# Kernel optimization log

Hardware: AMD Instinct MI355X
Metric: run time of the kernel (lower is better)

Reference implementation:

```python
import math
import jax, jax.numpy as jnp
import numpy as np

BLOCK = 32          # MRA block size (fixed to 32 by the CUDA kernels)
NUM_HEADS = 12
HEAD_DIM = 64
NUM_BLOCKS = 512    # top-k blocks kept per (batch*head) row
FIRST_N = 0         # initial_prior_first_n_blocks
DIAG_N = 3          # initial_prior_diagonal_n_blocks


def _low_res_logit(q, k, v, mask):
    # q,k,v: (B, S, D); mask: (B, S)
    B, S, D = q.shape
    nb = S // BLOCK
    tc = mask.reshape(B, nb, BLOCK).sum(-1)            # token count per block
    denom = tc[:, :, None] + 1e-6
    q_hat = q.reshape(B, nb, BLOCK, D).sum(2) / denom
    k_hat = k.reshape(B, nb, BLOCK, D).sum(2) / denom
    v_hat = v.reshape(B, nb, BLOCK, D).sum(2) / denom
    logit = jnp.einsum('bnd,bmd->bnm', q_hat, k_hat) / math.sqrt(D)
    row_max = logit.max(-1, keepdims=True)             # before mask penalty, as in torch
    logit = logit - 1e4 * ((tc[:, None, :] * tc[:, :, None]) < 0.5).astype(logit.dtype)
    return logit, tc, row_max, v_hat


def _block_idxes(lrl):
    # lrl: (B, nb, nb) normalized low-res logits (stop-gradient'ed by caller)
    B, nb, _ = lrl.shape
    if DIAG_N > 0:
        off = DIAG_N // 2
        r = jnp.arange(nb)
        diag = (jnp.abs(r[:, None] - r[None, :]) <= off).astype(lrl.dtype)
        lrl = lrl + diag[None] * 5000.0
    if FIRST_N > 0:
        lrl = lrl.at[:, :FIRST_N, :].add(5000.0)
        lrl = lrl.at[:, :, :FIRST_N].add(5000.0)
    vals, idx = jax.lax.top_k(lrl.reshape(B, -1), NUM_BLOCKS)
    thresh = vals.min(-1)
    hi_mask = (lrl >= thresh[:, None, None]).astype(lrl.dtype)
    return idx, hi_mask


def mra2_attention(q, k, v, mask):
    # q,k,v: (meta_batch, S, D); mask: (meta_batch, S). approx_mode == 'full'.
    B, S, D = q.shape
    nb = S // BLOCK
    q = q * mask[:, :, None]
    k = k * mask[:, :, None]
    v = v * mask[:, :, None]
    lrl, tc, row_max, v_hat = _low_res_logit(q, k, v, mask)
    idx, hi_mask = _block_idxes(jax.lax.stop_gradient(lrl - row_max))
    qi = idx // nb                                     # (B, NUM_BLOCKS) query block id
    ki = idx % nb                                      # (B, NUM_BLOCKS) key block id
    b_ix = jnp.arange(B)[:, None]
    # mm_to_sparse: gather blocks, block layout is (key_pos, query_pos) as in the CUDA kernel
    qb = q.reshape(B, nb, BLOCK, D)[b_ix, qi]          # (B, NB, 32, D)
    kb = k.reshape(B, nb, BLOCK, D)[b_ix, ki]
    hr_logit = jnp.einsum('bnkd,bnqd->bnkq', kb, qb) / math.sqrt(D)
    # sparse_max: per-query-row max over all selected blocks in that row
    idx_vals = hr_logit.max(-2)                        # (B, NB, 32q)
    max_vals = jnp.full((B, nb, BLOCK), -1e9, hr_logit.dtype).at[b_ix, qi].max(idx_vals)
    hr_logit = hr_logit - max_vals[b_ix, qi][:, :, None, :]
    # sparse_mask over key positions of each selected block
    mk = mask.reshape(B, nb, BLOCK)[b_ix, ki]          # (B, NB, 32k)
    hr_logit = hr_logit - 1e4 * (1.0 - mk)[:, :, :, None]
    hr_attn = jnp.exp(hr_logit)
    # sparse_dense_mm: scatter-add block contributions back to query rows
    vb = v.reshape(B, nb, BLOCK, D)[b_ix, ki]
    out_blk = jnp.einsum('bnkq,bnkd->bnqd', hr_attn, vb)
    hr_out = jnp.zeros((B, nb, BLOCK, D), q.dtype).at[b_ix, qi].add(out_blk).reshape(B, S, D)
    hr_norm = jnp.zeros((B, nb, BLOCK), q.dtype).at[b_ix, qi].add(hr_attn.sum(-2)).reshape(B, S)
    max_vals_flat = max_vals.reshape(B, S)
    # low-resolution branch (approx_mode == 'full')
    lr_attn = jnp.exp(lrl - row_max - 1e4 * hi_mask) * tc[:, None, :]
    lr_out = jnp.broadcast_to(
        jnp.einsum('bnm,bmd->bnd', lr_attn, v_hat)[:, :, None, :], (B, nb, BLOCK, D)
    ).reshape(B, S, D)
    lr_norm = jnp.broadcast_to(lr_attn.sum(-1)[:, :, None], (B, nb, BLOCK)).reshape(B, S)
    log_corr = (jnp.broadcast_to(row_max, (B, nb, BLOCK)).reshape(B, S) - max_vals_flat) * mask
    lr_corr = jnp.exp(log_corr * (log_corr <= 0).astype(log_corr.dtype))
    hr_corr = jnp.exp(-log_corr * (log_corr > 0).astype(log_corr.dtype))
    num = hr_out * hr_corr[:, :, None] + lr_out * lr_corr[:, :, None]
    den = hr_norm * hr_corr + lr_norm * lr_corr + 1e-6
    ctx = num / den[:, :, None]
    return ctx * mask[:, :, None]


def setup_inputs() -> dict:
    key = jax.random.key(0)
    ks = jax.random.split(key, 4)
    B, S, H = 4, 4096, 768
    return {
        'hidden_states': jax.random.normal(ks[0], (B, S, H), jnp.float32),
        'attention_mask': jnp.zeros((B, S), jnp.float32),  # extended mask form (0 == keep)
        'Wq': jax.random.normal(ks[1], (H, H), jnp.float32) * 0.02,
        'bq': jnp.zeros((H,), jnp.float32),
        'Wk': jax.random.normal(ks[2], (H, H), jnp.float32) * 0.02,
        'bk': jnp.zeros((H,), jnp.float32),
        'Wv': jax.random.normal(ks[3], (H, H), jnp.float32) * 0.02,
        'bv': jnp.zeros((H,), jnp.float32),
    }


def reference(hidden_states, attention_mask, Wq, bq, Wk, bk, Wv, bv):
    B, S, H = hidden_states.shape

    def heads(x):  # (B,S,H) -> (B*nh, S, hd)
        return x.reshape(B, S, NUM_HEADS, HEAD_DIM).transpose(0, 2, 1, 3).reshape(B * NUM_HEADS, S, HEAD_DIM)

    q = heads(hidden_states @ Wq.T + bq)
    k = heads(hidden_states @ Wk.T + bk)
    v = heads(hidden_states @ Wv.T + bv)
    # revert get_extended_attention_mask: (1 - m) * -10000 -> m
    mask = 1.0 + attention_mask / 10000.0
    mask = jnp.broadcast_to(mask[:, None, :], (B, NUM_HEADS, S)).reshape(B * NUM_HEADS, S)
    ctx = mra2_attention(q, k, v, mask)
    return ctx.reshape(B, NUM_HEADS, S, HEAD_DIM).transpose(0, 2, 1, 3).reshape(B, S, H)
```

## Files before the change

### kernel.cpp

```cpp
#include <hip/hip_runtime.h>
#include <math.h>


#define S_LEN 4096
#define NBLK  128
#define BHT   48
#define HD    64

typedef __attribute__((ext_vector_type(8))) short bf16x8;
typedef __attribute__((ext_vector_type(4))) float f32x4;
typedef unsigned short u16;
typedef unsigned int   u32;
typedef unsigned long long u64;

__device__ __forceinline__ u16 bf16rne(float x) {
    u32 u = __float_as_uint(x);
    u32 r = u + 0x7FFFu + ((u >> 16) & 1u);
    return (u16)(r >> 16);
}
__device__ __forceinline__ float b2f(u16 h) {
    return __uint_as_float((u32)h << 16);
}

__device__ __forceinline__ void gload_lds16(const void* g, void* l) {
    __builtin_amdgcn_global_load_lds((const __attribute__((address_space(1))) void*)g,
                                     (__attribute__((address_space(3))) void*)l, 16, 0, 0);
}

__global__ __launch_bounds__(256) void split_kernel(
    const float* __restrict__ x, u16* __restrict__ hi, u16* __restrict__ lo, int n8)
{
    int i = blockIdx.x * 256 + threadIdx.x;
    if (i >= n8) return;
    const float4* xp = (const float4*)x + (size_t)i * 2;
    float4 a = xp[0], b = xp[1];
    float xs[8] = {a.x, a.y, a.z, a.w, b.x, b.y, b.z, b.w};
    bf16x8 vh, vl;
    #pragma unroll
    for (int j = 0; j < 8; ++j) {
        u16 hh = bf16rne(xs[j]);
        float hf = b2f(hh);
        vh[j] = (short)hh;
        vl[j] = (short)bf16rne(xs[j] - hf);
    }
    *(bf16x8*)&hi[(size_t)i * 8] = vh;
    *(bf16x8*)&lo[(size_t)i * 8] = vl;
}

__global__ __launch_bounds__(256, 3) void qkv_mfma(
    const u16* __restrict__ Xh, const u16* __restrict__ Xl,
    const u16* __restrict__ Wh, const u16* __restrict__ Wl,
    const float* __restrict__ bq, const float* __restrict__ bk, const float* __restrict__ bv,
    const float* __restrict__ am,
    u16* __restrict__ Qh, u16* __restrict__ Ql,
    u16* __restrict__ Kh, u16* __restrict__ Kl,
    u16* __restrict__ Vth, u16* __restrict__ Vtl)
{
    const int wg = blockIdx.x;
    const int logical = (wg & 7) * 288 + (wg >> 3);
    const int mt = logical / 18;
    const int rr = logical - mt * 18;
    const int nt = rr % 6;
    const int z  = rr / 6;

    const float* bias = (z == 0) ? bq : (z == 1) ? bk : bv;
    const u16* Wzh = Wh + (size_t)z * 768 * 768;
    const u16* Wzl = Wl + (size_t)z * 768 * 768;
    const int m0 = mt * 128, n0 = nt * 128;

    __shared__ char smem[16896];
    const int tid  = threadIdx.x;
    const int lane = tid & 63;
    const int w    = tid >> 6;
    const int wm   = (w >> 1) * 64, wn = (w & 1) * 64;

    const int rbase = (w < 2) ? m0 : n0;
    const int sub0  = (w & 1) * 4;
    char* ldsdst    = (w < 2) ? smem : (smem + 8192);
    const int srow = lane >> 2;
    const int scg  = (lane & 3) ^ ((lane >> 3) & 3);
    const int tslot = (lane & 15) * 4 + ((lane >> 4) ^ ((lane >> 1) & 3));

    f32x4 acc[4][4];
    #pragma unroll
    for (int i = 0; i < 4; ++i)
        #pragma unroll
        for (int j = 0; j < 4; ++j) acc[i][j] = (f32x4){0.f, 0.f, 0.f, 0.f};

    for (int k0 = 0; k0 < 2304; k0 += 32) {
        const u16* srcA = (k0 < 1536) ? Xh : Xl;
        const u16* srcB = (k0 < 768) ? Wzh : ((k0 < 1536) ? Wzl : Wzh);
        const int  kk   = (k0 < 768) ? k0 : ((k0 < 1536) ? (k0 - 768) : (k0 - 1536));
        const u16* src  = (w < 2) ? srcA : srcB;
        __syncthreads();
        #pragma unroll
        for (int i = 0; i < 4; ++i) {
            const u16* g = src + (size_t)(rbase + (sub0 + i) * 16 + srow) * 768 + (kk + scg * 8);
            gload_lds16(g, ldsdst + (sub0 + i) * 1024);
        }
        __syncthreads();

        bf16x8 af[4], bf[4];
        #pragma unroll
        for (int f = 0; f < 4; ++f) {
            af[f] = *(const bf16x8*)&smem[0    + ((w >> 1) * 4 + f) * 1024 + tslot * 16];
            bf[f] = *(const bf16x8*)&smem[8192 + ((w & 1)  * 4 + f) * 1024 + tslot * 16];
        }
        #pragma unroll
        for (int i = 0; i < 4; ++i)
            #pragma unroll
            for (int j = 0; j < 4; ++j)
                acc[i][j] = __builtin_amdgcn_mfma_f32_16x16x32_bf16(af[i], bf[j], acc[i][j], 0, 0, 0);
    }

    if (z < 2) {
        u16* Ph = (z == 0) ? Qh : Kh;
        u16* Pl = (z == 0) ? Ql : Kl;
        const float qscale = (z == 0) ? 0.125f : 1.0f;
        #pragma unroll
        for (int i = 0; i < 4; ++i) {
            #pragma unroll
            for (int j = 0; j < 4; ++j) {
                int col = n0 + wn + j * 16 + (lane & 15);
                int h = col >> 6, d = col & 63;
                float bsv = bias[col];
                #pragma unroll
                for (int r = 0; r < 4; ++r) {
                    int row = m0 + wm + i * 16 + (lane >> 4) * 4 + r;
                    int b = row >> 12, s = row & 4095;
                    float mv = 1.0f + am[row] * 1e-4f;
                    float e = (acc[i][j][r] + bsv) * mv * qscale;
                    u16 hh = bf16rne(e);
                    u16 ll = bf16rne(e - b2f(hh));
                    size_t a = (((size_t)(b * 12 + h)) * S_LEN + s) * HD + d;
                    Ph[a] = hh; Pl[a] = ll;
                }
            }
        }
    } else {
        u32* buf = (u32*)smem;
        const int bb = m0 >> 12;
        #pragma unroll
        for (int p = 0; p < 4; ++p) {
            const int hh_ = p & 1;
            const int rh  = p >> 1;
            __syncthreads();
            if (((w & 1) == hh_) && ((w >> 1) == rh)) {
                #pragma unroll
                for (int i = 0; i < 4; ++i) {
                    #pragma unroll
                    for (int j = 0; j < 4; ++j) {
                        int d_local = j * 16 + (lane & 15);
                        int col = n0 + hh_ * 64 + d_local;
                        float bsv = bias[col];
                        #pragma unroll
                        for (int r = 0; r < 4; ++r) {
                            int s_local = i * 16 + (lane >> 4) * 4 + r;
                            float mv = 1.0f + am[m0 + rh * 64 + s_local] * 1e-4f;
                            float e = (acc[i][j][r] + bsv) * mv;
                            u16 h16 = bf16rne(e);
                            u16 l16 = bf16rne(e - b2f(h16));
                            buf[d_local * 66 + s_local] = ((u32)h16 << 16) | (u32)l16;
                        }
                    }
                }
            }
            __syncthreads();
            int d_local = tid >> 2;
            int s_chunk = (tid & 3) * 16;
            int head = (n0 >> 6) + hh_;
            size_t ob = (((size_t)(bb * 12 + head)) * HD + d_local) * S_LEN
                        + (m0 & 4095) + rh * 64 + s_chunk;
            #pragma unroll
            for (int gq = 0; gq < 2; ++gq) {
                bf16x8 vh8, vl8;
                #pragma unroll
                for (int t = 0; t < 8; ++t) {
                    u32 pk = buf[d_local * 66 + s_chunk + gq * 8 + t];
                    vh8[t] = (short)(pk >> 16);
                    vl8[t] = (short)(pk & 0xFFFF);
                }
                *(bf16x8*)&Vth[ob + gq * 8] = vh8;
                *(bf16x8*)&Vtl[ob + gq * 8] = vl8;
            }
        }
    }
}

__global__ __launch_bounds__(256) void hsum_kernel(
    const float* __restrict__ X, const float* __restrict__ am,
    double* __restrict__ hsum, double* __restrict__ tcd)
{
    int blk = blockIdx.x & 127, b = blockIdx.x >> 7;
    int tid = threadIdx.x;
    const float* xb  = X  + ((size_t)(b * S_LEN + blk * 32)) * 768;
    const float* amb = am + b * S_LEN + blk * 32;
    for (int d = tid; d < 768; d += 256) {
        double s = 0.0;
        for (int t = 0; t < 32; ++t)
            s += (double)xb[(size_t)t * 768 + d] * (1.0 + (double)amb[t] * 1e-4);
        hsum[(size_t)blockIdx.x * 768 + d] = s;
    }
    if (tid == 0) {
        double t = 0.0;
        for (int i = 0; i < 32; ++i) t += 1.0 + (double)amb[i] * 1e-4;
        tcd[blockIdx.x] = t;
    }
}

__global__ __launch_bounds__(256) void ghat_kernel(
    const double* __restrict__ hsum,
    const float* __restrict__ Wq, const float* __restrict__ Wk,
    const float* __restrict__ bq, const float* __restrict__ bk,
    const double* __restrict__ tcd,
    double* __restrict__ qhat, double* __restrict__ khat)
{
    const float* W; const float* bias; double* outp;
    if (blockIdx.z == 0) { W = Wq; bias = bq; outp = qhat; }
    else                 { W = Wk; bias = bk; outp = khat; }
    const int n0 = blockIdx.x * 64, m0 = blockIdx.y * 64;
    __shared__ double As[16][72];
    __shared__ float  Bs[16][72];
    const int tid = threadIdx.x;
    const int tx = tid & 15, ty = tid >> 4;
    double acc[4][4] = {};
    const int lr = tid >> 2, lc = (tid & 3) * 4;
    for (int k0 = 0; k0 < 768; k0 += 16) {
        double a0 = hsum[(size_t)(m0 + lr) * 768 + k0 + lc + 0];
        double a1 = hsum[(size_t)(m0 + lr) * 768 + k0 + lc + 1];
        double a2 = hsum[(size_t)(m0 + lr) * 768 + k0 + lc + 2];
        double a3 = hsum[(size_t)(m0 + lr) * 768 + k0 + lc + 3];
        float4 bv = *(const float4*)&W[(size_t)(n0 + lr) * 768 + k0 + lc];
        __syncthreads();
        As[lc+0][lr] = a0; As[lc+1][lr] = a1; As[lc+2][lr] = a2; As[lc+3][lr] = a3;
        Bs[lc+0][lr] = bv.x; Bs[lc+1][lr] = bv.y; Bs[lc+2][lr] = bv.z; Bs[lc+3][lr] = bv.w;
        __syncthreads();
        #pragma unroll
        for (int kk = 0; kk < 16; ++kk) {
            double af[4]; float bf[4];
            #pragma unroll
            for (int i = 0; i < 4; ++i) af[i] = As[kk][ty*4+i];
            #pragma unroll
            for (int j = 0; j < 4; ++j) bf[j] = Bs[kk][tx*4+j];
            #pragma unroll
            for (int i = 0; i < 4; ++i)
                #pragma unroll
                for (int j = 0; j < 4; ++j)
                    acc[i][j] += af[i] * (double)bf[j];
        }
    }
    #pragma unroll
    for (int i = 0; i < 4; ++i) {
        int m = m0 + ty*4 + i;
        int b = m >> 7, blk = m & 127;
        double t = tcd[m];
        #pragma unroll
        for (int j = 0; j < 4; ++j) {
            int o = n0 + tx*4 + j;
            int h = o >> 6, d = o & 63;
            outp[(((size_t)(b*12 + h)) * NBLK + blk) * HD + d] = (acc[i][j] + t * (double)bias[o]) / (t + 1e-6);
        }
    }
}

__global__ __launch_bounds__(128) void lrl_kernel(
    const double* __restrict__ qhat, const double* __restrict__ khat,
    const double* __restrict__ tcd,
    double* __restrict__ lrl, double* __restrict__ rmax)
{
    const int qi = blockIdx.x, bh = blockIdx.y;
    const int b = bh / 12;
    __shared__ double qr[64];
    __shared__ double red[128];
    const int tid = threadIdx.x;
    if (tid < 64) qr[tid] = qhat[(((size_t)bh) * NBLK + qi) * HD + tid];
    __syncthreads();
    const double* kr = &khat[(((size_t)bh) * NBLK + tid) * HD];
    double s = 0.0;
    for (int d = 0; d < 64; ++d) s += qr[d] * kr[d];
    s *= 0.125;
    red[tid] = s;
    __syncthreads();
    for (int off = 64; off > 0; off >>= 1) {
        if (tid < off) red[tid] = fmax(red[tid], red[tid + off]);
        __syncthreads();
    }
    double pen = (tcd[b * NBLK + qi] * tcd[b * NBLK + tid] < 0.5) ? 1e4 : 0.0;
    lrl[(size_t)bh * (NBLK*NBLK) + (size_t)qi * NBLK + tid] = s - pen;
    if (tid == 0) rmax[bh * NBLK + qi] = red[0];
}

__global__ __launch_bounds__(64) void vhat_kernel(
    const u16* __restrict__ Vth, const u16* __restrict__ Vtl, const float* __restrict__ am,
    float* __restrict__ vhat, float* __restrict__ tcf)
{
    int blk = blockIdx.x & 127, bh = blockIdx.x >> 7;
    int b = bh / 12;
    int d = threadIdx.x;
    const float* amb = am + b * S_LEN + blk * 32;
    float tc = 0.f;
    for (int t = 0; t < 32; ++t) tc += 1.0f + amb[t] * 1e-4f;
    float s = 0.f;
    size_t base = (((size_t)bh) * HD + d) * S_LEN + blk * 32;
    for (int t = 0; t < 32; ++t) s += b2f(Vth[base + t]) + b2f(Vtl[base + t]);
    vhat[(((size_t)bh) * NBLK + blk) * HD + d] = s / (tc + 1e-6f);
    if (d == 0) tcf[bh * NBLK + blk] = tc;
}

__device__ __forceinline__ u64 sel_key(const double* lp, const double* rm, int i)
{
    int qi = i >> 7, ki = i & 127;
    double s = lp[i] - rm[qi];
    int dd = qi - ki; if (dd < 0) dd = -dd;
    if (dd <= 1) s += 5000.0;
    u64 u = (u64)__double_as_longlong(s);
    u = (u >> 63) ? ~u : (u | 0x8000000000000000ULL);
    return u;
}

__global__ __launch_bounds__(256) void keys_kernel(
    const double* __restrict__ lrl, const double* __restrict__ rmax,
    u64* __restrict__ keys)
{
    const int bh = blockIdx.y;
    const int i = blockIdx.x * 256 + threadIdx.x;
    keys[(size_t)bh * (NBLK*NBLK) + i] =
        sel_key(lrl + (size_t)bh * (NBLK*NBLK), rmax + bh * NBLK, i);
}

__global__ __launch_bounds__(256) void topk_kernel(
    const u64* __restrict__ keys,
    double* __restrict__ th64, int* __restrict__ cnt, unsigned char* __restrict__ lists,
    int* __restrict__ eqbuf, int* __restrict__ eqcnt)
{
    const int bh = blockIdx.x, tid = threadIdx.x;
    __shared__ int hist[256];
    __shared__ u64 s_pref;
    __shared__ int s_K;
    const u64* kp = keys + (size_t)bh * (NBLK*NBLK);
    if (tid < 128) cnt[bh * NBLK + tid] = 0;
    if (tid == 0) eqcnt[bh] = 0;

    u64 pref = 0, pmask = 0;
    int K = 512;
    for (int by = 7; by >= 0; --by) {
        hist[tid] = 0;
        __syncthreads();
        for (int i = tid; i < NBLK*NBLK; i += 256) {
            u64 u = kp[i];
            if ((u & pmask) == pref)
                atomicAdd(&hist[(int)((u >> (by*8)) & 255)], 1);
        }
        __syncthreads();
        if (tid == 0) {
            int c = 0, bsel = 0;
            for (int x = 255; x >= 0; --x) {
                if (c + hist[x] >= K) { bsel = x; break; }
                c += hist[x];
            }
            s_pref = pref | ((u64)bsel << (by*8));
            s_K = K - c;
        }
        __syncthreads();
        pref = s_pref; K = s_K;
        pmask |= 0xFFULL << (by*8);
        __syncthreads();
    }
    const u64 tkey = pref;
    int n_take = K;
    if (tid == 0) {
        u64 u = (tkey & 0x8000000000000000ULL) ? (tkey ^ 0x8000000000000000ULL) : ~tkey;
        th64[bh] = __longlong_as_double((long long)u);
    }
    for (int i = tid; i < NBLK*NBLK; i += 256) {
        u64 u = kp[i];
        if (u > tkey) {
            int qi = i >> 7, ki = i & 127;
            int pos = atomicAdd(&cnt[bh * NBLK + qi], 1);
            lists[(((size_t)bh) * NBLK + qi) * NBLK + pos] = (unsigned char)ki;
        } else if (u == tkey) {
            int e = atomicAdd(&eqcnt[bh], 1);
            if (e < 512) eqbuf[bh * 512 + e] = i;
        }
    }
    __syncthreads();
    if (tid == 0) {
        int ne = eqcnt[bh]; if (ne > 512) ne = 512;
        int* eb = &eqbuf[bh * 512];
        for (int a = 1; a < ne; ++a) {
            int v = eb[a]; int x = a - 1;
            while (x >= 0 && eb[x] > v) { eb[x+1] = eb[x]; --x; }
            eb[x+1] = v;
        }
        if (n_take > ne) n_take = ne;
        for (int j = 0; j < n_take; ++j) {
            int i = eb[j]; int qi = i >> 7, ki = i & 127;
            int pos = cnt[bh * NBLK + qi]++;
            lists[(((size_t)bh) * NBLK + qi) * NBLK + pos] = (unsigned char)ki;
        }
    }
    __syncthreads();
    if (tid < 128) {
        int n = cnt[bh * NBLK + tid];
        unsigned char* l = &lists[(((size_t)bh) * NBLK + tid) * NBLK];
        for (int a = 1; a < n; ++a) {
            unsigned char v = l[a]; int x = a - 1;
            while (x >= 0 && l[x] > v) { l[x+1] = l[x]; --x; }
            l[x+1] = v;
        }
    }
}

__global__ __launch_bounds__(64) void hr_mfma(
    const u16* __restrict__ Qh, const u16* __restrict__ Ql,
    const u16* __restrict__ Kh, const u16* __restrict__ Kl,
    const u16* __restrict__ Vth, const u16* __restrict__ Vtl,
    const double* __restrict__ lrl64, const double* __restrict__ rmax64, const double* __restrict__ th64,
    const int* __restrict__ cnt, const unsigned char* __restrict__ lists,
    const float* __restrict__ vhat, const float* __restrict__ tcf,
    const float* __restrict__ am, float* __restrict__ out)
{
    const int qi = blockIdx.x, bh = blockIdx.y;
    const int l  = threadIdx.x;
    const int lr_ = l & 15, lg = l >> 4;
    __shared__ u16 PhL[32][40];
    __shared__ u16 PlL[32][40];
    __shared__ float wlr[128];
    __shared__ float lrvec[64];

    bf16x8 qfh[2][2], qfl[2][2];
    #pragma unroll
    for (int qs = 0; qs < 2; ++qs)
        #pragma unroll
        for (int ds = 0; ds < 2; ++ds) {
            size_t a = (((size_t)bh) * S_LEN + qi * 32 + qs * 16 + lr_) * HD + ds * 32 + lg * 8;
            qfh[qs][ds] = *(const bf16x8*)&Qh[a];
            qfl[qs][ds] = *(const bf16x8*)&Ql[a];
        }

    float m_run[2][4], l_run[2][4];
    f32x4 oacc[2][4];
    #pragma unroll
    for (int qs = 0; qs < 2; ++qs) {
        #pragma unroll
        for (int r = 0; r < 4; ++r) { m_run[qs][r] = -1e30f; l_run[qs][r] = 0.f; }
        #pragma unroll
        for (int dv = 0; dv < 4; ++dv) oacc[qs][dv] = (f32x4){0.f, 0.f, 0.f, 0.f};
    }

    const int c = cnt[bh * NBLK + qi];
    const unsigned char* ml = &lists[(((size_t)bh) * NBLK + qi) * NBLK];

    for (int bi = 0; bi < c; ++bi) {
        const int ki = ml[bi];
        bf16x8 kfh[2][2], kfl[2][2];
        #pragma unroll
        for (int ks = 0; ks < 2; ++ks)
            #pragma unroll
            for (int ds = 0; ds < 2; ++ds) {
                size_t a = (((size_t)bh) * S_LEN + ki * 32 + ks * 16 + lr_) * HD + ds * 32 + lg * 8;
                kfh[ks][ds] = *(const bf16x8*)&Kh[a];
                kfl[ks][ds] = *(const bf16x8*)&Kl[a];
            }
        f32x4 S[2][2];
        #pragma unroll
        for (int qs = 0; qs < 2; ++qs)
            #pragma unroll
            for (int ks = 0; ks < 2; ++ks) S[qs][ks] = (f32x4){0.f, 0.f, 0.f, 0.f};
        #pragma unroll
        for (int ds = 0; ds < 2; ++ds)
            #pragma unroll
            for (int qs = 0; qs < 2; ++qs)
                #pragma unroll
                for (int ks = 0; ks < 2; ++ks) {
                    S[qs][ks] = __builtin_amdgcn_mfma_f32_16x16x32_bf16(qfh[qs][ds], kfh[ks][ds], S[qs][ks], 0, 0, 0);
                    S[qs][ks] = __builtin_amdgcn_mfma_f32_16x16x32_bf16(qfh[qs][ds], kfl[ks][ds], S[qs][ks], 0, 0, 0);
                    S[qs][ks] = __builtin_amdgcn_mfma_f32_16x16x32_bf16(qfl[qs][ds], kfh[ks][ds], S[qs][ks], 0, 0, 0);
                }
        float sc_[2][4];
        #pragma unroll
        for (int qs = 0; qs < 2; ++qs)
            #pragma unroll
            for (int r = 0; r < 4; ++r) {
                float bm = fmaxf(S[qs][0][r], S[qs][1][r]);
                bm = fmaxf(bm, __shfl_xor(bm, 1));
                bm = fmaxf(bm, __shfl_xor(bm, 2));
                bm = fmaxf(bm, __shfl_xor(bm, 4));
                bm = fmaxf(bm, __shfl_xor(bm, 8));
                float mn = fmaxf(m_run[qs][r], bm);
                sc_[qs][r] = expf(m_run[qs][r] - mn);
                m_run[qs][r] = mn;
            }
        #pragma unroll
        for (int qs = 0; qs < 2; ++qs) {
            #pragma unroll
            for (int r = 0; r < 4; ++r) {
                float p0 = expf(S[qs][0][r] - m_run[qs][r]);
                float p1 = expf(S[qs][1][r] - m_run[qs][r]);
                float rs = p0 + p1;
                rs += __shfl_xor(rs, 1);
                rs += __shfl_xor(rs, 2);
                rs += __shfl_xor(rs, 4);
                rs += __shfl_xor(rs, 8);
                l_run[qs][r] = l_run[qs][r] * sc_[qs][r] + rs;
                int row = qs * 16 + lg * 4 + r;
                u16 h0 = bf16rne(p0); u16 lo0 = bf16rne(p0 - b2f(h0));
                u16 h1 = bf16rne(p1); u16 lo1 = bf16rne(p1 - b2f(h1));
                PhL[row][lr_]      = h0;  PlL[row][lr_]      = lo0;
                PhL[row][16 + lr_] = h1;  PlL[row][16 + lr_] = lo1;
            }
            #pragma unroll
            for (int dv = 0; dv < 4; ++dv)
                #pragma unroll
                for (int r = 0; r < 4; ++r)
                    oacc[qs][dv][r] *= sc_[qs][r];
        }
        __syncthreads();
        bf16x8 pah[2], pal[2];
        #pragma unroll
        for (int qs = 0; qs < 2; ++qs) {
            pah[qs] = *(const bf16x8*)&PhL[qs * 16 + lr_][lg * 8];
            pal[qs] = *(const bf16x8*)&PlL[qs * 16 + lr_][lg * 8];
        }
        bf16x8 vfh[4], vfl[4];
        #pragma unroll
        for (int dv = 0; dv < 4; ++dv) {
            size_t a = (((size_t)bh) * HD + dv * 16 + lr_) * S_LEN + ki * 32 + lg * 8;
            vfh[dv] = *(const bf16x8*)&Vth[a];
            vfl[dv] = *(const bf16x8*)&Vtl[a];
        }
        #pragma unroll
        for (int qs = 0; qs < 2; ++qs)
            #pragma unroll
            for (int dv = 0; dv < 4; ++dv) {
                oacc[qs][dv] = __builtin_amdgcn_mfma_f32_16x16x32_bf16(pah[qs], vfh[dv], oacc[qs][dv], 0, 0, 0);
                oacc[qs][dv] = __builtin_amdgcn_mfma_f32_16x16x32_bf16(pah[qs], vfl[dv], oacc[qs][dv], 0, 0, 0);
                oacc[qs][dv] = __builtin_amdgcn_mfma_f32_16x16x32_bf16(pal[qs], vfh[dv], oacc[qs][dv], 0, 0, 0);
            }
        __syncthreads();
    }

    const double thv  = th64[bh];
    const double rm64 = rmax64[bh * NBLK + qi];
    const int b = bh / 12, h = bh % 12;
    float wpair = 0.f;
    #pragma unroll
    for (int half = 0; half < 2; ++half) {
        int m = l + half * 64;
        double lv = lrl64[(size_t)bh * (NBLK*NBLK) + (size_t)qi * NBLK + m];
        int dd = qi - m; if (dd < 0) dd = -dd;
        double s = lv - rm64 + ((dd <= 1) ? 5000.0 : 0.0);
        float wv;
        if (s >= thv) wv = 0.f;
        else          wv = (float)exp(lv - rm64) * tcf[bh * NBLK + m];
        wlr[m] = wv;
        wpair += wv;
    }
    float s_lrn = wpair;
    s_lrn += __shfl_xor(s_lrn, 1);
    s_lrn += __shfl_xor(s_lrn, 2);
    s_lrn += __shfl_xor(s_lrn, 4);
    s_lrn += __shfl_xor(s_lrn, 8);
    s_lrn += __shfl_xor(s_lrn, 16);
    s_lrn += __shfl_xor(s_lrn, 32);
    __syncthreads();
    float a_ = 0.f;
    for (int m = 0; m < 128; ++m)
        a_ += wlr[m] * vhat[(((size_t)bh) * NBLK + m) * HD + l];
    lrvec[l] = a_;
    __syncthreads();
    float lv4[4];
    #pragma unroll
    for (int dv = 0; dv < 4; ++dv) lv4[dv] = lrvec[dv * 16 + lr_];

    const float rmf = (float)rm64;
    #pragma unroll
    for (int qs = 0; qs < 2; ++qs)
        #pragma unroll
        for (int r = 0; r < 4; ++r) {
            int q = qs * 16 + lg * 4 + r;
            int srow = qi * 32 + q;
            float mv = 1.0f + am[b * S_LEN + srow] * 1e-4f;
            float logc = (rmf - m_run[qs][r]) * mv;
            float lrc = (logc <= 0.f) ? expf(logc)  : 1.0f;
            float hrc = (logc >  0.f) ? expf(-logc) : 1.0f;
            float den = l_run[qs][r] * hrc + s_lrn * lrc + 1e-6f;
            float scd = mv / den;
            size_t ob = ((size_t)(b * S_LEN + srow)) * 768 + h * HD;
            #pragma unroll
            for (int dv = 0; dv < 4; ++dv)
                out[ob + dv * 16 + lr_] = (oacc[qs][dv][r] * hrc + lv4[dv] * lrc) * scd;
        }
}

extern "C" void kernel_launch(void* const* d_in, const int* in_sizes, int n_in,
                              void* d_out, int out_size, void* d_ws, size_t ws_size,
                              hipStream_t stream)
{
    (void)in_sizes; (void)n_in; (void)out_size; (void)ws_size;
    const float* X  = (const float*)d_in[0];
    const float* am = (const float*)d_in[1];
    const float* Wq = (const float*)d_in[2];
    const float* bq = (const float*)d_in[3];
    const float* Wk = (const float*)d_in[4];
    const float* bk = (const float*)d_in[5];
    const float* Wv = (const float*)d_in[6];
    const float* bv = (const float*)d_in[7];
    float* out = (float*)d_out;

    char* p = (char*)d_ws;
    const size_t PLANE = (size_t)BHT * S_LEN * HD * 2;
    u16* Qh  = (u16*)p; p += PLANE;
    u16* Ql  = (u16*)p; p += PLANE;
    u16* Kh  = (u16*)p; p += PLANE;
    u16* Kl  = (u16*)p; p += PLANE;
    u16* Vth = (u16*)p; p += PLANE;
    u16* Vtl = (u16*)p; p += PLANE;
    char* region = p;

    char* pa = region;
    u16* Xh = (u16*)pa; pa += (size_t)16384 * 768 * 2;
    u16* Xl = (u16*)pa; pa += (size_t)16384 * 768 * 2;
    u16* Wh = (u16*)pa; pa += (size_t)3 * 768 * 768 * 2;
    u16* Wl = (u16*)pa; pa += (size_t)3 * 768 * 768 * 2;

    char* pb = region;
    double* hsum   = (double*)pb; pb += (size_t)512 * 768 * 8;
    double* tcd    = (double*)pb; pb += (size_t)512 * 8;
    double* qhat64 = (double*)pb; pb += (size_t)BHT * NBLK * HD * 8;
    double* khat64 = (double*)pb; pb += (size_t)BHT * NBLK * HD * 8;
    double* lrl64  = (double*)pb; pb += (size_t)BHT * NBLK * NBLK * 8;
    double* rmax64 = (double*)pb; pb += (size_t)BHT * NBLK * 8;
    double* th64   = (double*)pb; pb += (size_t)BHT * 8;
    u64* keys   = (u64*)pb;   pb += (size_t)BHT * NBLK * NBLK * 8;
    float* vhat = (float*)pb; pb += (size_t)BHT * NBLK * HD * 4;
    float* tcf  = (float*)pb; pb += (size_t)BHT * NBLK * 4;
    int* cnt    = (int*)pb;   pb += (size_t)BHT * NBLK * 4;
    int* eqbuf  = (int*)pb;   pb += (size_t)BHT * 512 * 4;
    int* eqcnt  = (int*)pb;   pb += (size_t)BHT * 4;
    unsigned char* lists = (unsigned char*)pb; pb += (size_t)BHT * NBLK * NBLK;

    split_kernel<<<6144, 256, 0, stream>>>(X, Xh, Xl, 16384 * 768 / 8);
    split_kernel<<<288, 256, 0, stream>>>(Wq, Wh + (size_t)0*768*768, Wl + (size_t)0*768*768, 768 * 768 / 8);
    split_kernel<<<288, 256, 0, stream>>>(Wk, Wh + (size_t)1*768*768, Wl + (size_t)1*768*768, 768 * 768 / 8);
    split_kernel<<<288, 256, 0, stream>>>(Wv, Wh + (size_t)2*768*768, Wl + (size_t)2*768*768, 768 * 768 / 8);
    qkv_mfma<<<2304, 256, 0, stream>>>(Xh, Xl, Wh, Wl, bq, bk, bv, am,
                                       Qh, Ql, Kh, Kl, Vth, Vtl);

    hsum_kernel<<<512, 256, 0, stream>>>(X, am, hsum, tcd);
    ghat_kernel<<<dim3(12, 8, 2), 256, 0, stream>>>(hsum, Wq, Wk, bq, bk, tcd, qhat64, khat64);
    lrl_kernel<<<dim3(128, BHT), 128, 0, stream>>>(qhat64, khat64, tcd, lrl64, rmax64);
    vhat_kernel<<<BHT * NBLK, 64, 0, stream>>>(Vth, Vtl, am, vhat, tcf);
    keys_kernel<<<dim3(64, BHT), 256, 0, stream>>>(lrl64, rmax64, keys);
    topk_kernel<<<BHT, 256, 0, stream>>>(keys, th64, cnt, lists, eqbuf, eqcnt);

    hr_mfma<<<dim3(NBLK, BHT), 64, 0, stream>>>(Qh, Ql, Kh, Kl, Vth, Vtl,
                                                lrl64, rmax64, th64,
                                                cnt, lists, vhat, tcf, am, out);
}
```

Before: 721.4 us.

## Vectorize vhat and lrl loads, privatize topk histograms, interleave hr_mfma loads with MFMAs

vhat_kernel is remapped so each thread sums two contiguous 32-token blocks of one V row using 16-byte bf16x8 loads, and it reuses the precomputed token counts instead of re-reading the mask. lrl_kernel reads khat with double2 loads. topk_kernel keeps one histogram per wavefront to reduce LDS atomic contention, at the cost of an extra merge step and barrier. hr_mfma interleaves K/V fragment loads with their MFMAs and fuses the softmax rescale loops, aiming to lower register pressure and improve overlap, though this may limit how far ahead the loads can be issued.

```diff
diff --git a/kernel.cpp b/kernel.cpp
--- a/kernel.cpp
+++ b/kernel.cpp
@@ -277,7 +277,11 @@
     __syncthreads();
     const double* kr = &khat[(((size_t)bh) * NBLK + tid) * HD];
     double s = 0.0;
-    for (int d = 0; d < 64; ++d) s += qr[d] * kr[d];
+    #pragma unroll
+    for (int d = 0; d < 64; d += 2) {
+        double2 kv2 = *(const double2*)&kr[d];
+        s += qr[d] * kv2.x + qr[d + 1] * kv2.y;
+    }
     s *= 0.125;
     red[tid] = s;
     __syncthreads();
@@ -291,20 +295,34 @@
 }
 
 __global__ __launch_bounds__(64) void vhat_kernel(
-    const u16* __restrict__ Vth, const u16* __restrict__ Vtl, const float* __restrict__ am,
+    const u16* __restrict__ Vth, const u16* __restrict__ Vtl,
+    const double* __restrict__ tcd,
     float* __restrict__ vhat, float* __restrict__ tcf)
 {
-    int blk = blockIdx.x & 127, bh = blockIdx.x >> 7;
-    int b = bh / 12;
-    int d = threadIdx.x;
-    const float* amb = am + b * S_LEN + blk * 32;
-    float tc = 0.f;
-    for (int t = 0; t < 32; ++t) tc += 1.0f + amb[t] * 1e-4f;
-    float s = 0.f;
-    size_t base = (((size_t)bh) * HD + d) * S_LEN + blk * 32;
-    for (int t = 0; t < 32; ++t) s += b2f(Vth[base + t]) + b2f(Vtl[base + t]);
-    vhat[(((size_t)bh) * NBLK + blk) * HD + d] = s / (tc + 1e-6f);
-    if (d == 0) tcf[bh * NBLK + blk] = tc;
+    const int d = blockIdx.x, bh = blockIdx.y;
+    const int b = bh / 12;
+    const int l = threadIdx.x;
+    const u16* ph = Vth + ((size_t)bh * HD + d) * S_LEN + l * 64;
+    const u16* pl = Vtl + ((size_t)bh * HD + d) * S_LEN + l * 64;
+    float s[2] = {0.f, 0.f};
+    #pragma unroll
+    for (int g = 0; g < 2; ++g) {
+        #pragma unroll
+        for (int v = 0; v < 4; ++v) {
+            bf16x8 vh = *(const bf16x8*)&ph[g * 32 + v * 8];
+            bf16x8 vl = *(const bf16x8*)&pl[g * 32 + v * 8];
+            #pragma unroll
+            for (int j = 0; j < 8; ++j)
+                s[g] += b2f((u16)vh[j]) + b2f((u16)vl[j]);
+        }
+    }
+    #pragma unroll
+    for (int g = 0; g < 2; ++g) {
+        int blk = l * 2 + g;
+        float tc = (float)tcd[b * NBLK + blk];
+        vhat[(((size_t)bh) * NBLK + blk) * HD + d] = s[g] / (tc + 1e-6f);
+        if (d == 0) tcf[bh * NBLK + blk] = tc;
+    }
 }
 
 __device__ __forceinline__ u64 sel_key(const double* lp, const double* rm, int i)
@@ -334,7 +352,8 @@
     int* __restrict__ eqbuf, int* __restrict__ eqcnt)
 {
     const int bh = blockIdx.x, tid = threadIdx.x;
-    __shared__ int hist[256];
+    const int wid = tid >> 6;
+    __shared__ int hist[4][256];
     __shared__ u64 s_pref;
     __shared__ int s_K;
     const u64* kp = keys + (size_t)bh * (NBLK*NBLK);
@@ -344,19 +363,23 @@
     u64 pref = 0, pmask = 0;
     int K = 512;
     for (int by = 7; by >= 0; --by) {
-        hist[tid] = 0;
+        #pragma unroll
+        for (int w = 0; w < 4; ++w) hist[w][tid] = 0;
         __syncthreads();
         for (int i = tid; i < NBLK*NBLK; i += 256) {
             u64 u = kp[i];
             if ((u & pmask) == pref)
-                atomicAdd(&hist[(int)((u >> (by*8)) & 255)], 1);
-        }
+                atomicAdd(&hist[wid][(int)((u >> (by*8)) & 255)], 1);
+        }
+        __syncthreads();
+        int tot = hist[0][tid] + hist[1][tid] + hist[2][tid] + hist[3][tid];
+        hist[0][tid] = tot;
         __syncthreads();
         if (tid == 0) {
             int c = 0, bsel = 0;
             for (int x = 255; x >= 0; --x) {
-                if (c + hist[x] >= K) { bsel = x; break; }
-                c += hist[x];
+                if (c + hist[0][x] >= K) { bsel = x; break; }
+                c += hist[0][x];
             }
             s_pref = pref | ((u64)bsel << (by*8));
             s_K = K - c;
@@ -453,31 +476,25 @@
 
     for (int bi = 0; bi < c; ++bi) {
         const int ki = ml[bi];
-        bf16x8 kfh[2][2], kfl[2][2];
-        #pragma unroll
-        for (int ks = 0; ks < 2; ++ks)
-            #pragma unroll
-            for (int ds = 0; ds < 2; ++ds) {
+        f32x4 S[2][2];
+        #pragma unroll
+        for (int qs = 0; qs < 2; ++qs)
+            #pragma unroll
+            for (int ks = 0; ks < 2; ++ks) S[qs][ks] = (f32x4){0.f, 0.f, 0.f, 0.f};
+        #pragma unroll
+        for (int ds = 0; ds < 2; ++ds)
+            #pragma unroll
+            for (int ks = 0; ks < 2; ++ks) {
                 size_t a = (((size_t)bh) * S_LEN + ki * 32 + ks * 16 + lr_) * HD + ds * 32 + lg * 8;
-                kfh[ks][ds] = *(const bf16x8*)&Kh[a];
-                kfl[ks][ds] = *(const bf16x8*)&Kl[a];
+                bf16x8 kh = *(const bf16x8*)&Kh[a];
+                bf16x8 kl = *(const bf16x8*)&Kl[a];
+                S[0][ks] = __builtin_amdgcn_mfma_f32_16x16x32_bf16(qfh[0][ds], kh, S[0][ks], 0, 0, 0);
+                S[1][ks] = __builtin_amdgcn_mfma_f32_16x16x32_bf16(qfh[1][ds], kh, S[1][ks], 0, 0, 0);
+                S[0][ks] = __builtin_amdgcn_mfma_f32_16x16x32_bf16(qfh[0][ds], kl, S[0][ks], 0, 0, 0);
+                S[1][ks] = __builtin_amdgcn_mfma_f32_16x16x32_bf16(qfh[1][ds], kl, S[1][ks], 0, 0, 0);
+                S[0][ks] = __builtin_amdgcn_mfma_f32_16x16x32_bf16(qfl[0][ds], kh, S[0][ks], 0, 0, 0);
+                S[1][ks] = __builtin_amdgcn_mfma_f32_16x16x32_bf16(qfl[1][ds], kh, S[1][ks], 0, 0, 0);
             }
-        f32x4 S[2][2];
-        #pragma unroll
-        for (int qs = 0; qs < 2; ++qs)
-            #pragma unroll
-            for (int ks = 0; ks < 2; ++ks) S[qs][ks] = (f32x4){0.f, 0.f, 0.f, 0.f};
-        #pragma unroll
-        for (int ds = 0; ds < 2; ++ds)
-            #pragma unroll
-            for (int qs = 0; qs < 2; ++qs)
-                #pragma unroll
-                for (int ks = 0; ks < 2; ++ks) {
-                    S[qs][ks] = __builtin_amdgcn_mfma_f32_16x16x32_bf16(qfh[qs][ds], kfh[ks][ds], S[qs][ks], 0, 0, 0);
-                    S[qs][ks] = __builtin_amdgcn_mfma_f32_16x16x32_bf16(qfh[qs][ds], kfl[ks][ds], S[qs][ks], 0, 0, 0);
-                    S[qs][ks] = __builtin_amdgcn_mfma_f32_16x16x32_bf16(qfl[qs][ds], kfh[ks][ds], S[qs][ks], 0, 0, 0);
-                }
-        float sc_[2][4];
         #pragma unroll
         for (int qs = 0; qs < 2; ++qs)
             #pragma unroll
@@ -488,33 +505,24 @@
                 bm = fmaxf(bm, __shfl_xor(bm, 4));
                 bm = fmaxf(bm, __shfl_xor(bm, 8));
                 float mn = fmaxf(m_run[qs][r], bm);
-                sc_[qs][r] = expf(m_run[qs][r] - mn);
+                float sc = expf(m_run[qs][r] - mn);
                 m_run[qs][r] = mn;
-            }
-        #pragma unroll
-        for (int qs = 0; qs < 2; ++qs) {
-            #pragma unroll
-            for (int r = 0; r < 4; ++r) {
-                float p0 = expf(S[qs][0][r] - m_run[qs][r]);
-                float p1 = expf(S[qs][1][r] - m_run[qs][r]);
+                float p0 = expf(S[qs][0][r] - mn);
+                float p1 = expf(S[qs][1][r] - mn);
                 float rs = p0 + p1;
                 rs += __shfl_xor(rs, 1);
                 rs += __shfl_xor(rs, 2);
                 rs += __shfl_xor(rs, 4);
                 rs += __shfl_xor(rs, 8);
-                l_run[qs][r] = l_run[qs][r] * sc_[qs][r] + rs;
+                l_run[qs][r] = l_run[qs][r] * sc + rs;
+                #pragma unroll
+                for (int dv = 0; dv < 4; ++dv) oacc[qs][dv][r] *= sc;
                 int row = qs * 16 + lg * 4 + r;
                 u16 h0 = bf16rne(p0); u16 lo0 = bf16rne(p0 - b2f(h0));
                 u16 h1 = bf16rne(p1); u16 lo1 = bf16rne(p1 - b2f(h1));
                 PhL[row][lr_]      = h0;  PlL[row][lr_]      = lo0;
                 PhL[row][16 + lr_] = h1;  PlL[row][16 + lr_] = lo1;
             }
-            #pragma unroll
-            for (int dv = 0; dv < 4; ++dv)
-                #pragma unroll
-                for (int r = 0; r < 4; ++r)
-                    oacc[qs][dv][r] *= sc_[qs][r];
-        }
         __syncthreads();
         bf16x8 pah[2], pal[2];
         #pragma unroll
@@ -522,21 +530,18 @@
             pah[qs] = *(const bf16x8*)&PhL[qs * 16 + lr_][lg * 8];
             pal[qs] = *(const bf16x8*)&PlL[qs * 16 + lr_][lg * 8];
         }
-        bf16x8 vfh[4], vfl[4];
         #pragma unroll
         for (int dv = 0; dv < 4; ++dv) {
             size_t a = (((size_t)bh) * HD + dv * 16 + lr_) * S_LEN + ki * 32 + lg * 8;
-            vfh[dv] = *(const bf16x8*)&Vth[a];
-            vfl[dv] = *(const bf16x8*)&Vtl[a];
-        }
-        #pragma unroll
-        for (int qs = 0; qs < 2; ++qs)
-            #pragma unroll
-            for (int dv = 0; dv < 4; ++dv) {
-                oacc[qs][dv] = __builtin_amdgcn_mfma_f32_16x16x32_bf16(pah[qs], vfh[dv], oacc[qs][dv], 0, 0, 0);
-                oacc[qs][dv] = __builtin_amdgcn_mfma_f32_16x16x32_bf16(pah[qs], vfl[dv], oacc[qs][dv], 0, 0, 0);
-                oacc[qs][dv] = __builtin_amdgcn_mfma_f32_16x16x32_bf16(pal[qs], vfh[dv], oacc[qs][dv], 0, 0, 0);
+            bf16x8 vh = *(const bf16x8*)&Vth[a];
+            bf16x8 vl = *(const bf16x8*)&Vtl[a];
+            #pragma unroll
+            for (int qs = 0; qs < 2; ++qs) {
+                oacc[qs][dv] = __builtin_amdgcn_mfma_f32_16x16x32_bf16(pah[qs], vh, oacc[qs][dv], 0, 0, 0);
+                oacc[qs][dv] = __builtin_amdgcn_mfma_f32_16x16x32_bf16(pah[qs], vl, oacc[qs][dv], 0, 0, 0);
+                oacc[qs][dv] = __builtin_amdgcn_mfma_f32_16x16x32_bf16(pal[qs], vh, oacc[qs][dv], 0, 0, 0);
             }
+        }
         __syncthreads();
     }
 
@@ -650,7 +655,7 @@
     hsum_kernel<<<512, 256, 0, stream>>>(X, am, hsum, tcd);
     ghat_kernel<<<dim3(12, 8, 2), 256, 0, stream>>>(hsum, Wq, Wk, bq, bk, tcd, qhat64, khat64);
     lrl_kernel<<<dim3(128, BHT), 128, 0, stream>>>(qhat64, khat64, tcd, lrl64, rmax64);
-    vhat_kernel<<<BHT * NBLK, 64, 0, stream>>>(Vth, Vtl, am, vhat, tcf);
+    vhat_kernel<<<dim3(64, BHT), 64, 0, stream>>>(Vth, Vtl, tcd, vhat, tcf);
     keys_kernel<<<dim3(64, BHT), 256, 0, stream>>>(lrl64, rmax64, keys);
     topk_kernel<<<BHT, 256, 0, stream>>>(keys, th64, cnt, lists, eqbuf, eqcnt);
 
```

Result: no change. 725.5 us (+0.6%).
